# Performance work log

Measured on AMD Instinct MI355X. Metric: run time of the kernel, lower is better.

## Reference

```python
import jax, jax.numpy as jnp
import numpy as np

NUM_NODES = 16384
NUM_EDGES = 524288
D_IN = 128
D_OUT = 128


def setup_inputs() -> dict:
    key = jax.random.key(0)
    k1, k2, k3 = jax.random.split(key, 3)
    x = jax.random.normal(k1, (NUM_NODES, D_IN), dtype=jnp.float32)
    edge_index = jax.random.randint(k2, (2, NUM_EDGES), 0, NUM_NODES, dtype=jnp.int64)
    # Xavier-uniform-like W; B is zeros in the original init but we use small
    # random values so its branch contributes to the output numerically.
    limit = float(np.sqrt(6.0 / (D_IN + D_OUT)))
    W = jax.random.uniform(k3, (D_OUT, D_IN), dtype=jnp.float32, minval=-limit, maxval=limit)
    B = jax.random.normal(jax.random.fold_in(key, 7), (D_OUT, D_IN), dtype=jnp.float32) * 0.02
    return {"x": x, "edge_index": edge_index, "W": W, "B": B}


def reference(x, edge_index, W, B):
    n = x.shape[0]
    src = edge_index[0]
    dst = edge_index[1]
    # Dense adjacency: A[i, j] = 1 iff edge j -> i (duplicates collapse via set)
    A = jnp.zeros((n, n), dtype=x.dtype).at[dst, src].set(1.0)
    deg = A.sum(axis=1)                      # in-degree per node
    d_inv = 1.0 / jnp.maximum(deg, 1.0)      # clamp(min=1)
    agg = d_inv[:, None] * (A @ x)           # D_inv @ A @ x (diag as row scale)
    out = agg @ W.T + x @ B.T                # F.linear(.., W) + F.linear(x, B)
    return out
```

## Files before the change

### kernel.cpp

```cpp
#include <hip/hip_runtime.h>

#define NN  16384
#define NE  524288
#define D   128
#define CAP 128

#define OFF_CNT  0u
#define OFF_SLAB 65536u
#define OFF_Y    4259840u
#define OFF_Z    8454144u
#define OFF_XB   16842752u
#define OFF_WB   21037056u

typedef __bf16 bf16x4 __attribute__((ext_vector_type(4)));
typedef __bf16 bf16x8 __attribute__((ext_vector_type(8)));
typedef float  f32x4  __attribute__((ext_vector_type(4)));
typedef unsigned short u16;

__global__ __launch_bounds__(256) void prep_k(const float* __restrict__ x,
                                              const float* __restrict__ W,
                                              const float* __restrict__ Bm,
                                              __bf16* __restrict__ xb,
                                              __bf16* __restrict__ wbg,
                                              int4* __restrict__ cnt4) {
  int b = blockIdx.x, t = threadIdx.x;
  if (b < 16) {
    cnt4[b * 256 + t] = int4{0, 0, 0, 0};
  } else if (b < 48) {
    int i = (b - 16) * 256 + t;
    float4 v = (i < 4096) ? ((const float4*)W)[i] : ((const float4*)Bm)[i - 4096];
    bf16x4 w = {(__bf16)v.x, (__bf16)v.y, (__bf16)v.z, (__bf16)v.w};
    ((bf16x4*)wbg)[i] = w;
  } else {
    int i = (b - 48) * 256 + t;
    float4 v = ((const float4*)x)[i];
    bf16x4 w = {(__bf16)v.x, (__bf16)v.y, (__bf16)v.z, (__bf16)v.w};
    ((bf16x4*)xb)[i] = w;
  }
}

__global__ __launch_bounds__(256, 2) void k1(const u16* __restrict__ xb,
                                             const u16* __restrict__ wbg,
                                             const int* __restrict__ ei,
                                             __bf16* __restrict__ y,
                                             float* __restrict__ z,
                                             int* __restrict__ cnt,
                                             u16* __restrict__ slab) {
  __shared__ __align__(16) __bf16 swb[256][136];
  __shared__ int s_any;
  int b = blockIdx.x, t = threadIdx.x;

  if (b < 256) {
    int l = t & 63, wid = t >> 6;
    int g = l >> 4, ln = l & 15;
    int row0 = b * 64;

#pragma unroll
    for (int u = 0; u < 16; ++u) {
      int e = u * 256 + t;
      int rr = e >> 4, q = e & 15;
      uint4 v = ((const uint4*)wbg)[e];
      *(uint4*)&swb[rr][q * 8] = v;
    }
    __syncthreads();

    f32x4 accY[8], accZ[8];
#pragma unroll
    for (int nb = 0; nb < 8; ++nb) {
      accY[nb] = f32x4{0.f, 0.f, 0.f, 0.f};
      accZ[nb] = f32x4{0.f, 0.f, 0.f, 0.f};
    }
    const u16* xrow = xb + (size_t)(row0 + wid * 16 + ln) * D;

#pragma unroll
    for (int kc = 0; kc < 4; ++kc) {
      bf16x8 afr = *(const bf16x8*)(xrow + kc * 32 + g * 8);
#pragma unroll
      for (int nb = 0; nb < 8; ++nb) {
        bf16x8 bw = *(const bf16x8*)&swb[nb * 16 + ln][kc * 32 + g * 8];
        accY[nb] = __builtin_amdgcn_mfma_f32_16x16x32_bf16(afr, bw, accY[nb], 0, 0, 0);
        bf16x8 bb = *(const bf16x8*)&swb[128 + nb * 16 + ln][kc * 32 + g * 8];
        accZ[nb] = __builtin_amdgcn_mfma_f32_16x16x32_bf16(afr, bb, accZ[nb], 0, 0, 0);
      }
    }
#pragma unroll
    for (int nb = 0; nb < 8; ++nb)
#pragma unroll
      for (int i = 0; i < 4; ++i) {
        size_t orow = (size_t)(row0 + wid * 16 + g * 4 + i) * D + nb * 16 + ln;
        y[orow] = (__bf16)accY[nb][i];
        z[orow] = accZ[nb][i];
      }
  } else {
    if (t == 0) s_any = 0;
    __syncthreads();
    int base = (b - 256) * 2048;
    int any = 0;
#pragma unroll
    for (int u = 0; u < 8; ++u) any |= ei[2 * (base + u * 256 + t) + 1];
    if (any) atomicOr(&s_any, 1);
    __syncthreads();
    int is32 = s_any;
    int s_[8], d_[8], slot_[8];
#pragma unroll
    for (int u = 0; u < 8; ++u) {
      int i = base + u * 256 + t;
      s_[u] = is32 ? ei[i] : ei[2 * i];
      d_[u] = is32 ? ei[NE + i] : ei[2 * (NE + i)];
    }
#pragma unroll
    for (int u = 0; u < 8; ++u)
      slot_[u] = atomicAdd(&cnt[d_[u]], 1);
#pragma unroll
    for (int u = 0; u < 8; ++u)
      if (slot_[u] < CAP) slab[((size_t)d_[u] << 7) + slot_[u]] = (u16)s_[u];
  }
}

#define RPB 8
__global__ __launch_bounds__(256) void gather_k(const int* __restrict__ cnt,
                                                const u16* __restrict__ slab,
                                                const u16* __restrict__ y,
                                                const float* __restrict__ z,
                                                float* __restrict__ out) {
  __shared__ u16 s_col[RPB][CAP];
  __shared__ unsigned s_bm[RPB][512];
  int t = threadIdx.x, lane = t & 31, r = t >> 5;
  int row = blockIdx.x * RPB + r;
  float4 zv = *(const float4*)(z + (size_t)row * D + lane * 4);
  int k = cnt[row];
  if (k > CAP) k = CAP;
  const u16* srow = slab + ((size_t)row << 7);
  for (int j = lane; j < k; j += 32) s_col[r][j] = srow[j];
#pragma unroll
  for (int u = 0; u < 16; ++u) s_bm[r][u * 32 + lane] = 0u;

  int lu = 0;
  for (int j = lane; j < k; j += 32) {
    unsigned c = s_col[r][j];
    unsigned bit = 1u << (c & 31);
    unsigned old = atomicOr(&s_bm[r][c >> 5], bit);
    int kp = (old & bit) ? 0 : 1;
    s_col[r][j] = (u16)(c | (kp << 15));
    lu += kp;
  }
#pragma unroll
  for (int off = 16; off; off >>= 1) lu += __shfl_xor(lu, off);
  float dinv = 1.0f / (float)(lu > 0 ? lu : 1);

  float4 a[8];
#pragma unroll
  for (int u = 0; u < 8; ++u) a[u] = float4{0.f, 0.f, 0.f, 0.f};
  const u16* yl = y + lane * 4;
#define ACCB(aa, vv, ff)                                                  \
  { aa.x += ff * __uint_as_float((vv).x << 16);                           \
    aa.y += ff * __uint_as_float((vv).x & 0xffff0000u);                   \
    aa.z += ff * __uint_as_float((vv).y << 16);                           \
    aa.w += ff * __uint_as_float((vv).y & 0xffff0000u); }
  int j = 0;
  for (; j + 8 <= k; j += 8) {
    float f[8];
    uint2 v[8];
#pragma unroll
    for (int u = 0; u < 8; ++u) {
      int cc = s_col[r][j + u];
      f[u] = (cc >> 15) ? 1.0f : 0.0f;
      v[u] = *(const uint2*)(yl + (size_t)(cc & 0x3FFF) * D);
    }
#pragma unroll
    for (int u = 0; u < 8; ++u) ACCB(a[u], v[u], f[u])
  }
  for (; j < k; ++j) {
    int cc = s_col[r][j];
    float f0 = (cc >> 15) ? 1.0f : 0.0f;
    uint2 v0 = *(const uint2*)(yl + (size_t)(cc & 0x3FFF) * D);
    ACCB(a[0], v0, f0)
  }
#undef ACCB
#pragma unroll
  for (int u = 4; u < 8; ++u) {
    a[u - 4].x += a[u].x; a[u - 4].y += a[u].y;
    a[u - 4].z += a[u].z; a[u - 4].w += a[u].w;
  }
  float4 o;
  o.x = (a[0].x + a[1].x + a[2].x + a[3].x) * dinv + zv.x;
  o.y = (a[0].y + a[1].y + a[2].y + a[3].y) * dinv + zv.y;
  o.z = (a[0].z + a[1].z + a[2].z + a[3].z) * dinv + zv.z;
  o.w = (a[0].w + a[1].w + a[2].w + a[3].w) * dinv + zv.w;
  *(float4*)(out + (size_t)row * D + lane * 4) = o;
}

extern "C" void kernel_launch(void* const* d_in, const int* in_sizes, int n_in,
                              void* d_out, int out_size, void* d_ws, size_t ws_size,
                              hipStream_t stream) {
  const float* x = (const float*)d_in[0];
  const int* ei = (const int*)d_in[1];
  const float* W = (const float*)d_in[2];
  const float* Bm = (const float*)d_in[3];
  float* out = (float*)d_out;
  char* ws = (char*)d_ws;
  int* cnt = (int*)(ws + OFF_CNT);
  u16* slab = (u16*)(ws + OFF_SLAB);
  __bf16* y = (__bf16*)(ws + OFF_Y);
  float* z = (float*)(ws + OFF_Z);
  __bf16* xb = (__bf16*)(ws + OFF_XB);
  __bf16* wbg = (__bf16*)(ws + OFF_WB);

  prep_k<<<2096, 256, 0, stream>>>(x, W, Bm, xb, wbg, (int4*)cnt);
  k1<<<512, 256, 0, stream>>>((const u16*)xb, (const u16*)wbg, ei, y, z, cnt, slab);
  gather_k<<<NN / RPB, 256, 0, stream>>>(cnt, slab, (const u16*)y, z, out);
}
```

Baseline: 58.34 us.

## Fuse bf16 conversion into GEMM and shard per-destination edge counters four ways

The x/W/B fp32-to-bf16 conversion moves out of the prep kernel and into the GEMM blocks, which now read fp32 directly and convert in registers. This drops the xb/wbg intermediate round-trip and leaves the prep kernel only zeroing counters. The edge bucketing atomics are split into four sub-counters per destination (by edge index mod 4), each with a 32-slot sub-slab, to reduce atomic contention on hot destinations. The gather kernel concatenates the four sub-lists, at the cost of extra count reads and a per-shard capacity that can overflow sooner than the old single 128-slot cap.

```diff
diff --git a/kernel.cpp b/kernel.cpp
--- a/kernel.cpp
+++ b/kernel.cpp
@@ -3,44 +3,25 @@
 #define NN  16384
 #define NE  524288
 #define D   128
-#define CAP 128
+#define SCAP 32
 
 #define OFF_CNT  0u
-#define OFF_SLAB 65536u
-#define OFF_Y    4259840u
-#define OFF_Z    8454144u
-#define OFF_XB   16842752u
-#define OFF_WB   21037056u
+#define OFF_SLAB 262144u
+#define OFF_Y    4456448u
+#define OFF_Z    8650752u
 
 typedef __bf16 bf16x4 __attribute__((ext_vector_type(4)));
 typedef __bf16 bf16x8 __attribute__((ext_vector_type(8)));
 typedef float  f32x4  __attribute__((ext_vector_type(4)));
 typedef unsigned short u16;
 
-__global__ __launch_bounds__(256) void prep_k(const float* __restrict__ x,
-                                              const float* __restrict__ W,
-                                              const float* __restrict__ Bm,
-                                              __bf16* __restrict__ xb,
-                                              __bf16* __restrict__ wbg,
-                                              int4* __restrict__ cnt4) {
-  int b = blockIdx.x, t = threadIdx.x;
-  if (b < 16) {
-    cnt4[b * 256 + t] = int4{0, 0, 0, 0};
-  } else if (b < 48) {
-    int i = (b - 16) * 256 + t;
-    float4 v = (i < 4096) ? ((const float4*)W)[i] : ((const float4*)Bm)[i - 4096];
-    bf16x4 w = {(__bf16)v.x, (__bf16)v.y, (__bf16)v.z, (__bf16)v.w};
-    ((bf16x4*)wbg)[i] = w;
-  } else {
-    int i = (b - 48) * 256 + t;
-    float4 v = ((const float4*)x)[i];
-    bf16x4 w = {(__bf16)v.x, (__bf16)v.y, (__bf16)v.z, (__bf16)v.w};
-    ((bf16x4*)xb)[i] = w;
-  }
-}
-
-__global__ __launch_bounds__(256, 2) void k1(const u16* __restrict__ xb,
-                                             const u16* __restrict__ wbg,
+__global__ __launch_bounds__(256) void prep_k(int4* __restrict__ cnt4) {
+  cnt4[blockIdx.x * 256 + threadIdx.x] = int4{0, 0, 0, 0};
+}
+
+__global__ __launch_bounds__(256, 2) void k1(const float* __restrict__ x,
+                                             const float* __restrict__ W,
+                                             const float* __restrict__ Bm,
                                              const int* __restrict__ ei,
                                              __bf16* __restrict__ y,
                                              float* __restrict__ z,
@@ -59,8 +40,13 @@
     for (int u = 0; u < 16; ++u) {
       int e = u * 256 + t;
       int rr = e >> 4, q = e & 15;
-      uint4 v = ((const uint4*)wbg)[e];
-      *(uint4*)&swb[rr][q * 8] = v;
+      const float* src = (rr < 128) ? &W[(size_t)rr * D + q * 8]
+                                    : &Bm[(size_t)(rr - 128) * D + q * 8];
+      float4 v0 = *(const float4*)src;
+      float4 v1 = *(const float4*)(src + 4);
+      bf16x8 w = {(__bf16)v0.x, (__bf16)v0.y, (__bf16)v0.z, (__bf16)v0.w,
+                  (__bf16)v1.x, (__bf16)v1.y, (__bf16)v1.z, (__bf16)v1.w};
+      *(bf16x8*)&swb[rr][q * 8] = w;
     }
     __syncthreads();
 
@@ -70,11 +56,14 @@
       accY[nb] = f32x4{0.f, 0.f, 0.f, 0.f};
       accZ[nb] = f32x4{0.f, 0.f, 0.f, 0.f};
     }
-    const u16* xrow = xb + (size_t)(row0 + wid * 16 + ln) * D;
+    const float* xrow = x + (size_t)(row0 + wid * 16 + ln) * D;
 
 #pragma unroll
     for (int kc = 0; kc < 4; ++kc) {
-      bf16x8 afr = *(const bf16x8*)(xrow + kc * 32 + g * 8);
+      float4 a0 = *(const float4*)(xrow + kc * 32 + g * 8);
+      float4 a1 = *(const float4*)(xrow + kc * 32 + g * 8 + 4);
+      bf16x8 afr = {(__bf16)a0.x, (__bf16)a0.y, (__bf16)a0.z, (__bf16)a0.w,
+                    (__bf16)a1.x, (__bf16)a1.y, (__bf16)a1.z, (__bf16)a1.w};
 #pragma unroll
       for (int nb = 0; nb < 8; ++nb) {
         bf16x8 bw = *(const bf16x8*)&swb[nb * 16 + ln][kc * 32 + g * 8];
@@ -101,19 +90,21 @@
     if (any) atomicOr(&s_any, 1);
     __syncthreads();
     int is32 = s_any;
-    int s_[8], d_[8], slot_[8];
+    int s_[8], d_[8], slot_[8], sh_[8];
 #pragma unroll
     for (int u = 0; u < 8; ++u) {
       int i = base + u * 256 + t;
       s_[u] = is32 ? ei[i] : ei[2 * i];
       d_[u] = is32 ? ei[NE + i] : ei[2 * (NE + i)];
+      sh_[u] = i & 3;
     }
 #pragma unroll
     for (int u = 0; u < 8; ++u)
-      slot_[u] = atomicAdd(&cnt[d_[u]], 1);
+      slot_[u] = atomicAdd(&cnt[d_[u] * 4 + sh_[u]], 1);
 #pragma unroll
     for (int u = 0; u < 8; ++u)
-      if (slot_[u] < CAP) slab[((size_t)d_[u] << 7) + slot_[u]] = (u16)s_[u];
+      if (slot_[u] < SCAP)
+        slab[((size_t)d_[u] << 7) + sh_[u] * SCAP + slot_[u]] = (u16)s_[u];
   }
 }
 
@@ -123,15 +114,23 @@
                                                 const u16* __restrict__ y,
                                                 const float* __restrict__ z,
                                                 float* __restrict__ out) {
-  __shared__ u16 s_col[RPB][CAP];
+  __shared__ u16 s_col[RPB][128];
   __shared__ unsigned s_bm[RPB][512];
   int t = threadIdx.x, lane = t & 31, r = t >> 5;
   int row = blockIdx.x * RPB + r;
   float4 zv = *(const float4*)(z + (size_t)row * D + lane * 4);
-  int k = cnt[row];
-  if (k > CAP) k = CAP;
+  int4 c4 = *(const int4*)(cnt + row * 4);
+  int cs[4] = {c4.x, c4.y, c4.z, c4.w};
+#pragma unroll
+  for (int s = 0; s < 4; ++s) cs[s] = cs[s] > SCAP ? SCAP : cs[s];
   const u16* srow = slab + ((size_t)row << 7);
-  for (int j = lane; j < k; j += 32) s_col[r][j] = srow[j];
+  int kbase = 0;
+#pragma unroll
+  for (int s = 0; s < 4; ++s) {
+    for (int j = lane; j < cs[s]; j += 32) s_col[r][kbase + j] = srow[s * SCAP + j];
+    kbase += cs[s];
+  }
+  int k = kbase;
 #pragma unroll
   for (int u = 0; u < 16; ++u) s_bm[r][u * 32 + lane] = 0u;
 
@@ -203,10 +202,8 @@
   u16* slab = (u16*)(ws + OFF_SLAB);
   __bf16* y = (__bf16*)(ws + OFF_Y);
   float* z = (float*)(ws + OFF_Z);
-  __bf16* xb = (__bf16*)(ws + OFF_XB);
-  __bf16* wbg = (__bf16*)(ws + OFF_WB);
-
-  prep_k<<<2096, 256, 0, stream>>>(x, W, Bm, xb, wbg, (int4*)cnt);
-  k1<<<512, 256, 0, stream>>>((const u16*)xb, (const u16*)wbg, ei, y, z, cnt, slab);
+
+  prep_k<<<64, 256, 0, stream>>>((int4*)cnt);
+  k1<<<512, 256, 0, stream>>>(x, W, Bm, ei, y, z, cnt, slab);
   gather_k<<<NN / RPB, 256, 0, stream>>>(cnt, slab, (const u16*)y, z, out);
 }
```

Measured after the change: 61.06 us. 4.6% more time.
